# Kernel optimization log

Hardware: AMD Instinct MI355X
Metric: run time of the kernel (lower is better)

The kernel has to match this reference:

```python
import jax, jax.numpy as jnp
import numpy as np

HH, WW = 7, 7  # pooled output size (module init: height, width)


def setup_inputs() -> dict:
    key = jax.random.key(0)
    k1, k2, k3, k4, k5 = jax.random.split(key, 5)
    C, Hf, Wf = 512, 64, 256        # conv feature map (stride 8)
    B = 4096                        # number of RoI boxes
    img_h, img_w = 512, 2048        # original image size
    feats = jax.random.normal(k1, (C, Hf, Wf), dtype=jnp.float32)
    w = jax.random.uniform(k2, (B,), minval=16.0, maxval=256.0)
    h = jax.random.uniform(k3, (B,), minval=16.0, maxval=128.0)
    xc = jax.random.uniform(k4, (B,), minval=0.0, maxval=float(img_w))
    yc = jax.random.uniform(k5, (B,), minval=0.0, maxval=float(img_h))
    boxes = jnp.stack([xc, yc, w, h], axis=1).astype(jnp.float32)  # (B,4) xc,yc,w,h in image coords
    return {"feats": feats, "boxes": boxes, "img_height": img_h, "img_width": img_w}


def _bilinear_sample(feats, px, py):
    """feats: (C,Hf,Wf); px,py: (B,HH,WW) pixel coords in feature map. Zero padding outside."""
    C, Hf, Wf = feats.shape
    x0 = jnp.floor(px)
    y0 = jnp.floor(py)
    x1 = x0 + 1.0
    y1 = y0 + 1.0
    wx1 = px - x0
    wx0 = 1.0 - wx1
    wy1 = py - y0
    wy0 = 1.0 - wy1

    def gather(xi, yi):
        valid = (xi >= 0) & (xi <= Wf - 1) & (yi >= 0) & (yi <= Hf - 1)
        xi_c = jnp.clip(xi, 0, Wf - 1).astype(jnp.int32)
        yi_c = jnp.clip(yi, 0, Hf - 1).astype(jnp.int32)
        v = feats[:, yi_c, xi_c]                     # (C,B,HH,WW)
        return v * valid[None].astype(feats.dtype)

    out = (gather(x0, y0) * (wx0 * wy0)[None]
           + gather(x1, y0) * (wx1 * wy0)[None]
           + gather(x0, y1) * (wx0 * wy1)[None]
           + gather(x1, y1) * (wx1 * wy1)[None])    # (C,B,HH,WW)
    return jnp.transpose(out, (1, 0, 2, 3))          # (B,C,HH,WW)


def reference(feats, boxes, img_height, img_width):
    # box_to_affine (densecap BoxToAffine, align_corners=True normalization) fused
    # with affine_grid: sample coords computed inline per box.
    B = boxes.shape[0]
    C, Hf, Wf = feats.shape
    xc, yc, w, h = boxes[:, 0], boxes[:, 1], boxes[:, 2], boxes[:, 3]
    tx = jnp.linspace(-1.0, 1.0, WW, dtype=feats.dtype)
    ty = jnp.linspace(-1.0, 1.0, HH, dtype=feats.dtype)
    inv_w = 1.0 / (img_width - 1)
    inv_h = 1.0 / (img_height - 1)
    # normalized image coords: gx = (2*xc-(W-1))/(W-1) + tx * w/(W-1)
    gx = (2.0 * xc[:, None] - (img_width - 1)) * inv_w + (w * inv_w)[:, None] * tx[None, :]   # (B,WW)
    gy = (2.0 * yc[:, None] - (img_height - 1)) * inv_h + (h * inv_h)[:, None] * ty[None, :]  # (B,HH)
    # map normalized [-1,1] to feature-map pixel coords (align_corners=True)
    px = (gx + 1.0) * 0.5 * (Wf - 1)
    py = (gy + 1.0) * 0.5 * (Hf - 1)
    px = jnp.broadcast_to(px[:, None, :], (B, HH, WW))
    py = jnp.broadcast_to(py[:, :, None], (B, HH, WW))
    return _bilinear_sample(feats, px, py)            # (B,C,HH,WW)
```

## Files before the change

### kernel.cpp

```cpp
#include <hip/hip_runtime.h>
#include <math.h>

#define HH 7
#define WW 7
#define CC 512
#define HF 64
#define WF 256
#define NS 49
#define CHUNK 128
#define ROWS4 (CC / 4)
#define NE4 ((CHUNK * NS) / 4)
#define NBINS 2048

typedef float floatv4 __attribute__((ext_vector_type(4)));

__global__ __launch_bounds__(256) void transpose_feats(const float* __restrict__ in,
                                                       float* __restrict__ out) {
    __shared__ float tile[32][33];
    const int P = HF * WF;
    int p  = blockIdx.x * 32 + threadIdx.x;
    int cb = blockIdx.y * 32;
#pragma unroll
    for (int r = 0; r < 32; r += 8)
        tile[threadIdx.y + r][threadIdx.x] = in[(size_t)(cb + threadIdx.y + r) * P + p];
    __syncthreads();
    int c  = cb + threadIdx.x;
    int pb = blockIdx.x * 32;
#pragma unroll
    for (int r = 0; r < 32; r += 8)
        out[(size_t)(pb + threadIdx.y + r) * CC + c] = tile[threadIdx.x][threadIdx.y + r];
}

__device__ __forceinline__ int box_key(const float* __restrict__ boxes, int b,
                                       float sy, float sx) {
    float xc = boxes[b * 4 + 0];
    float yc = boxes[b * 4 + 1];
    int yb = (int)(yc * sy);
    int xb = (int)(xc * sx);
    yb = min(max(yb, 0), 31);
    xb = min(max(xb, 0), 63);
    if (yb & 1) xb = 63 - xb;
    return (yb << 6) | xb;
}

__global__ __launch_bounds__(256) void sort_boxes(const float* __restrict__ boxes,
                                                  const int* __restrict__ ih_p,
                                                  const int* __restrict__ iw_p,
                                                  int B, int* __restrict__ perm) {
    __shared__ int hist[NBINS];
    __shared__ int part[256];
    const int tid = threadIdx.x;
    const float sy = 32.0f / (float)ih_p[0];
    const float sx = 64.0f / (float)iw_p[0];

    for (int i = tid; i < NBINS; i += 256) hist[i] = 0;
    __syncthreads();
    for (int b = tid; b < B; b += 256)
        atomicAdd(&hist[box_key(boxes, b, sy, sx)], 1);
    __syncthreads();
    const int base = tid * (NBINS / 256);
    int s = 0;
#pragma unroll
    for (int i = 0; i < NBINS / 256; ++i) { int v = hist[base + i]; hist[base + i] = s; s += v; }
    part[tid] = s;
    __syncthreads();
    if (tid == 0) {
        int acc = 0;
        for (int t = 0; t < 256; ++t) { int v = part[t]; part[t] = acc; acc += v; }
    }
    __syncthreads();
    const int off = part[tid];
#pragma unroll
    for (int i = 0; i < NBINS / 256; ++i) hist[base + i] += off;
    __syncthreads();
    for (int b = tid; b < B; b += 256) {
        int pos = atomicAdd(&hist[box_key(boxes, b, sy, sx)], 1);
        perm[pos] = b;
    }
}

__device__ __forceinline__ void box_setup(int s, int b,
                                          const float* __restrict__ boxes,
                                          const int* __restrict__ ih_p,
                                          const int* __restrict__ iw_p,
                                          int4* o_out, float4* w_out) {
    int i = s / WW;
    int j = s - i * WW;
    float IW1 = (float)(iw_p[0] - 1);
    float IH1 = (float)(ih_p[0] - 1);
    float xc = boxes[b * 4 + 0];
    float yc = boxes[b * 4 + 1];
    float bw = boxes[b * 4 + 2];
    float bh = boxes[b * 4 + 3];
    float inv_w = 1.0f / IW1;
    float inv_h = 1.0f / IH1;
    float tx = (float)(j - 3) * (1.0f / 3.0f);
    float ty = (float)(i - 3) * (1.0f / 3.0f);
    float gx = (2.0f * xc - IW1) * inv_w + (bw * inv_w) * tx;
    float gy = (2.0f * yc - IH1) * inv_h + (bh * inv_h) * ty;
    float px = (gx + 1.0f) * 0.5f * (float)(WF - 1);
    float py = (gy + 1.0f) * 0.5f * (float)(HF - 1);

    float x0f = floorf(px), y0f = floorf(py);
    float wx1 = px - x0f, wx0 = 1.0f - wx1;
    float wy1 = py - y0f, wy0 = 1.0f - wy1;
    float x1f = x0f + 1.0f, y1f = y0f + 1.0f;

    bool vx0 = (x0f >= 0.0f) && (x0f <= (float)(WF - 1));
    bool vx1 = (x1f >= 0.0f) && (x1f <= (float)(WF - 1));
    bool vy0 = (y0f >= 0.0f) && (y0f <= (float)(HF - 1));
    bool vy1 = (y1f >= 0.0f) && (y1f <= (float)(HF - 1));

    int xi0 = (int)fminf(fmaxf(x0f, 0.0f), (float)(WF - 1));
    int xi1 = (int)fminf(fmaxf(x1f, 0.0f), (float)(WF - 1));
    int yi0 = (int)fminf(fmaxf(y0f, 0.0f), (float)(HF - 1));
    int yi1 = (int)fminf(fmaxf(y1f, 0.0f), (float)(HF - 1));

    int4 o;
    o.x = yi0 * WF + xi0;
    o.y = yi0 * WF + xi1;
    o.z = yi1 * WF + xi0;
    o.w = yi1 * WF + xi1;
    float4 w4;
    w4.x = wx0 * wy0 * ((vx0 && vy0) ? 1.0f : 0.0f);
    w4.y = wx1 * wy0 * ((vx1 && vy0) ? 1.0f : 0.0f);
    w4.z = wx0 * wy1 * ((vx0 && vy1) ? 1.0f : 0.0f);
    w4.w = wx1 * wy1 * ((vx1 && vy1) ? 1.0f : 0.0f);
    *o_out = o;
    *w_out = w4;
}

__global__ __launch_bounds__(256) void roi_pool_v4(const float* __restrict__ src,
                                                   const float* __restrict__ boxes,
                                                   const int* __restrict__ ih_p,
                                                   const int* __restrict__ iw_p,
                                                   const int* __restrict__ perm,
                                                   float* __restrict__ out) {
    __shared__ int4   s_off[NS];
    __shared__ float4 s_wt[NS];
    __shared__ float  tile[CHUNK * 64];

    const int nwg  = gridDim.x;
    const int bid  = blockIdx.x;
    const int q    = nwg >> 3, r = nwg & 7;
    const int xcd  = bid & 7, slot = bid >> 3;
    const int rank = xcd * q + min(xcd, r) + slot;
    const int b    = perm[rank];

    const int tid = threadIdx.x;
    const int g   = tid & 31;
    const int h   = tid >> 5;

    if (tid < NS) {
        int4 o; float4 w4;
        box_setup(tid, b, boxes, ih_p, iw_p, &o, &w4);
        o.x *= ROWS4; o.y *= ROWS4; o.z *= ROWS4; o.w *= ROWS4;
        s_off[tid] = o;
        s_wt[tid]  = w4;
    }
    __syncthreads();

    int4   o_r[7];
    float4 w_r[7];
    int    sig_r[7];
#pragma unroll
    for (int it = 0; it < 7; ++it) {
        int s = h + (it << 3);
        if (s < NS) {
            o_r[it]   = s_off[s];
            w_r[it]   = s_wt[s];
            sig_r[it] = (s >> 2) | ((s & 3) << 4);
        }
    }

    const size_t outbase = (size_t)b * (CC * NS);
    const float4* src4   = (const float4*)src;

    for (int c0 = 0; c0 < CC; c0 += CHUNK) {
        const int cb4 = c0 >> 2;
#pragma unroll
        for (int it = 0; it < 7; ++it) {
            int s = h + (it << 3);
            if (s < NS) {
                int4   o = o_r[it];
                float4 w = w_r[it];
                float4 a  = src4[o.x + cb4 + g];
                float4 bb = src4[o.y + cb4 + g];
                float4 c  = src4[o.z + cb4 + g];
                float4 d  = src4[o.w + cb4 + g];
                int base = g << 8;
                int sw   = sig_r[it] ^ g;
                tile[base +       sw] = a.x * w.x + bb.x * w.y + c.x * w.z + d.x * w.w;
                tile[base +  64 + sw] = a.y * w.x + bb.y * w.y + c.y * w.z + d.y * w.w;
                tile[base + 128 + sw] = a.z * w.x + bb.z * w.y + c.z * w.z + d.z * w.w;
                tile[base + 192 + sw] = a.w * w.x + bb.w * w.y + c.w * w.z + d.w * w.w;
            }
        }
        __syncthreads();
        float* outc = out + outbase + (size_t)c0 * NS;
        for (int k4 = tid; k4 < NE4; k4 += 256) {
            int e = k4 << 2;
            int c = e / NS;
            int s = e - c * NS;
            floatv4 v;
            v.x = tile[(c << 6) + (((s >> 2) | ((s & 3) << 4)) ^ (c >> 2))];
            if (++s == NS) { s = 0; ++c; }
            v.y = tile[(c << 6) + (((s >> 2) | ((s & 3) << 4)) ^ (c >> 2))];
            if (++s == NS) { s = 0; ++c; }
            v.z = tile[(c << 6) + (((s >> 2) | ((s & 3) << 4)) ^ (c >> 2))];
            if (++s == NS) { s = 0; ++c; }
            v.w = tile[(c << 6) + (((s >> 2) | ((s & 3) << 4)) ^ (c >> 2))];
            __builtin_nontemporal_store(v, (floatv4*)outc + k4);
        }
        __syncthreads();
    }
}

__global__ __launch_bounds__(256) void roi_pool_fb(const float* __restrict__ src,
                                                   const float* __restrict__ boxes,
                                                   const int* __restrict__ ih_p,
                                                   const int* __restrict__ iw_p,
                                                   float* __restrict__ out) {
    __shared__ int4   s_off[NS];
    __shared__ float4 s_wt[NS];
    __shared__ float  tile[NS * 257];

    const int b   = blockIdx.x;
    const int tid = threadIdx.x;

    if (tid < NS) {
        int4 o; float4 w4;
        box_setup(tid, b, boxes, ih_p, iw_p, &o, &w4);
        s_off[tid] = o;
        s_wt[tid]  = w4;
    }
    __syncthreads();

    const size_t outbase = (size_t)b * (CC * NS);
    for (int c0 = 0; c0 < CC; c0 += 256) {
        const int cterm = (c0 + tid) * (HF * WF);
        for (int s = 0; s < NS; ++s) {
            int4   o = s_off[s];
            float4 w = s_wt[s];
            float v = src[o.x + cterm] * w.x + src[o.y + cterm] * w.y +
                      src[o.z + cterm] * w.z + src[o.w + cterm] * w.w;
            tile[s * 257 + tid] = v;
        }
        __syncthreads();
        const size_t ob = outbase + (size_t)c0 * NS;
        for (int k = tid; k < 256 * NS; k += 256) {
            int cl = k / NS;
            int s  = k - cl * NS;
            out[ob + k] = tile[s * 257 + cl];
        }
        __syncthreads();
    }
}

extern "C" void kernel_launch(void* const* d_in, const int* in_sizes, int n_in,
                              void* d_out, int out_size, void* d_ws, size_t ws_size,
                              hipStream_t stream) {
    const float* feats = (const float*)d_in[0];
    const float* boxes = (const float*)d_in[1];
    const int*   ih    = (const int*)d_in[2];
    const int*   iw    = (const int*)d_in[3];
    float*       out   = (float*)d_out;
    const int B = in_sizes[1] / 4;

    const size_t tf_bytes = (size_t)CC * HF * WF * sizeof(float);
    const size_t need = tf_bytes + (size_t)B * sizeof(int);
    if (ws_size >= need) {
        float* tf   = (float*)d_ws;
        int*   perm = (int*)((char*)d_ws + tf_bytes);
        dim3 tb(32, 8);
        dim3 tg((HF * WF) / 32, CC / 32);
        transpose_feats<<<tg, tb, 0, stream>>>(feats, tf);
        sort_boxes<<<1, 256, 0, stream>>>(boxes, ih, iw, B, perm);
        roi_pool_v4<<<B, 256, 0, stream>>>(tf, boxes, ih, iw, perm, out);
    } else {
        roi_pool_fb<<<B, 256, 0, stream>>>(feats, boxes, ih, iw, out);
    }
}
```

Before: 473.5 us.

## Deduplicate bilinear source cells per box and stage them in LDS

The pooling kernel now computes the separable x/y sample coordinates once per axis, sorts and dedups the distinct feature rows and columns, and loads each unique (y,x) cell's channel vector into LDS only once per 32-channel chunk. Each output element is then interpolated from LDS using per-sample cell indices and weights, instead of issuing four global gathers per sample. This cuts redundant global loads when samples share neighbouring pixels, at the cost of extra serial setup (insertion sorts on single threads), more LDS reads per output and more barrier-separated chunks. The sort kernel's serial prefix over partial sums is also replaced with a parallel Hillis-Steele scan.

```diff
diff --git a/kernel.cpp b/kernel.cpp
--- a/kernel.cpp
+++ b/kernel.cpp
@@ -7,9 +7,10 @@
 #define HF 64
 #define WF 256
 #define NS 49
-#define CHUNK 128
-#define ROWS4 (CC / 4)
-#define NE4 ((CHUNK * NS) / 4)
+#define MAXC 196
+#define CSTR 40
+#define CH 32
+#define NP4 ((CH * NS) / 4)
 #define NBINS 2048
 
 typedef float floatv4 __attribute__((ext_vector_type(4)));
@@ -64,12 +65,13 @@
     for (int i = 0; i < NBINS / 256; ++i) { int v = hist[base + i]; hist[base + i] = s; s += v; }
     part[tid] = s;
     __syncthreads();
-    if (tid == 0) {
-        int acc = 0;
-        for (int t = 0; t < 256; ++t) { int v = part[t]; part[t] = acc; acc += v; }
-    }
-    __syncthreads();
-    const int off = part[tid];
+    for (int d = 1; d < 256; d <<= 1) {
+        int v = (tid >= d) ? part[tid - d] : 0;
+        __syncthreads();
+        part[tid] += v;
+        __syncthreads();
+    }
+    const int off = part[tid] - s;
 #pragma unroll
     for (int i = 0; i < NBINS / 256; ++i) hist[base + i] += off;
     __syncthreads();
@@ -130,15 +132,20 @@
     *w_out = w4;
 }
 
-__global__ __launch_bounds__(256) void roi_pool_v4(const float* __restrict__ src,
+__global__ __launch_bounds__(256) void roi_pool_v5(const float* __restrict__ src,
                                                    const float* __restrict__ boxes,
                                                    const int* __restrict__ ih_p,
                                                    const int* __restrict__ iw_p,
                                                    const int* __restrict__ perm,
                                                    float* __restrict__ out) {
-    __shared__ int4   s_off[NS];
+    __shared__ int    xs_l[14], ys_l[14];
+    __shared__ int    rx_l[7][2], ry_l[7][2];
+    __shared__ float  wxf[7][2], wyf[7][2];
+    __shared__ int    s_nx, s_ny;
+    __shared__ int    cell_off4[MAXC];
+    __shared__ int4   s_kq[NS];
     __shared__ float4 s_wt[NS];
-    __shared__ float  tile[CHUNK * 64];
+    __shared__ float  cell_lds[MAXC * CSTR];
 
     const int nwg  = gridDim.x;
     const int bid  = blockIdx.x;
@@ -146,70 +153,135 @@
     const int xcd  = bid & 7, slot = bid >> 3;
     const int rank = xcd * q + min(xcd, r) + slot;
     const int b    = perm[rank];
-
-    const int tid = threadIdx.x;
-    const int g   = tid & 31;
-    const int h   = tid >> 5;
+    const int tid  = threadIdx.x;
+
+    if (tid < 7) {
+        float IW1 = (float)(iw_p[0] - 1);
+        float IH1 = (float)(ih_p[0] - 1);
+        float xc = boxes[b * 4 + 0], yc = boxes[b * 4 + 1];
+        float bw = boxes[b * 4 + 2], bh = boxes[b * 4 + 3];
+        float t  = (float)(tid - 3) * (1.0f / 3.0f);
+
+        float gx  = (2.0f * xc - IW1) / IW1 + (bw / IW1) * t;
+        float px  = (gx + 1.0f) * 0.5f * (float)(WF - 1);
+        float x0f = floorf(px);
+        float wx1 = px - x0f, wx0 = 1.0f - wx1;
+        bool vx0 = (x0f >= 0.0f) && (x0f <= (float)(WF - 1));
+        bool vx1 = (x0f + 1.0f >= 0.0f) && (x0f + 1.0f <= (float)(WF - 1));
+        int xi0 = (int)fminf(fmaxf(x0f, 0.0f), (float)(WF - 1));
+        int xi1 = (int)fminf(fmaxf(x0f + 1.0f, 0.0f), (float)(WF - 1));
+        xs_l[2 * tid] = xi0; xs_l[2 * tid + 1] = xi1;
+        rx_l[tid][0] = xi0;  rx_l[tid][1] = xi1;
+        wxf[tid][0] = wx0 * (vx0 ? 1.0f : 0.0f);
+        wxf[tid][1] = wx1 * (vx1 ? 1.0f : 0.0f);
+
+        float gy  = (2.0f * yc - IH1) / IH1 + (bh / IH1) * t;
+        float py  = (gy + 1.0f) * 0.5f * (float)(HF - 1);
+        float y0f = floorf(py);
+        float wy1v = py - y0f, wy0v = 1.0f - wy1v;
+        bool vy0 = (y0f >= 0.0f) && (y0f <= (float)(HF - 1));
+        bool vy1 = (y0f + 1.0f >= 0.0f) && (y0f + 1.0f <= (float)(HF - 1));
+        int yi0 = (int)fminf(fmaxf(y0f, 0.0f), (float)(HF - 1));
+        int yi1 = (int)fminf(fmaxf(y0f + 1.0f, 0.0f), (float)(HF - 1));
+        ys_l[2 * tid] = yi0; ys_l[2 * tid + 1] = yi1;
+        ry_l[tid][0] = yi0;  ry_l[tid][1] = yi1;
+        wyf[tid][0] = wy0v * (vy0 ? 1.0f : 0.0f);
+        wyf[tid][1] = wy1v * (vy1 ? 1.0f : 0.0f);
+    }
+    __syncthreads();
+
+    if (tid == 0) {
+        for (int a = 1; a < 14; ++a) { int v = xs_l[a]; int p2 = a;
+            while (p2 > 0 && xs_l[p2 - 1] > v) { xs_l[p2] = xs_l[p2 - 1]; --p2; }
+            xs_l[p2] = v; }
+        int m = 1;
+        for (int a = 1; a < 14; ++a) if (xs_l[a] != xs_l[m - 1]) xs_l[m++] = xs_l[a];
+        s_nx = m;
+    }
+    if (tid == 64) {
+        for (int a = 1; a < 14; ++a) { int v = ys_l[a]; int p2 = a;
+            while (p2 > 0 && ys_l[p2 - 1] > v) { ys_l[p2] = ys_l[p2 - 1]; --p2; }
+            ys_l[p2] = v; }
+        int m = 1;
+        for (int a = 1; a < 14; ++a) if (ys_l[a] != ys_l[m - 1]) ys_l[m++] = ys_l[a];
+        s_ny = m;
+    }
+    __syncthreads();
+    const int nx = s_nx, ny = s_ny;
+    const int nc = nx * ny;
+
+    if (tid < 7) {
+#pragma unroll
+        for (int d = 0; d < 2; ++d) {
+            int v = rx_l[tid][d]; int idx = 0;
+            for (int a = 0; a < nx; ++a) if (xs_l[a] == v) idx = a;
+            rx_l[tid][d] = idx;
+            v = ry_l[tid][d]; idx = 0;
+            for (int a = 0; a < ny; ++a) if (ys_l[a] == v) idx = a;
+            ry_l[tid][d] = idx;
+        }
+    }
+    for (int k = tid; k < nc; k += 256) {
+        int ky = k / nx, kx = k - ky * nx;
+        cell_off4[k] = (ys_l[ky] * WF + xs_l[kx]) * (CC / 4);
+    }
+    __syncthreads();
 
     if (tid < NS) {
-        int4 o; float4 w4;
-        box_setup(tid, b, boxes, ih_p, iw_p, &o, &w4);
-        o.x *= ROWS4; o.y *= ROWS4; o.z *= ROWS4; o.w *= ROWS4;
-        s_off[tid] = o;
-        s_wt[tid]  = w4;
-    }
-    __syncthreads();
-
-    int4   o_r[7];
-    float4 w_r[7];
-    int    sig_r[7];
-#pragma unroll
-    for (int it = 0; it < 7; ++it) {
-        int s = h + (it << 3);
-        if (s < NS) {
-            o_r[it]   = s_off[s];
-            w_r[it]   = s_wt[s];
-            sig_r[it] = (s >> 2) | ((s & 3) << 4);
-        }
-    }
+        int i = tid / 7, j = tid - i * 7;
+        int r0 = ry_l[i][0] * nx, r1 = ry_l[i][1] * nx;
+        int c0i = rx_l[j][0], c1i = rx_l[j][1];
+        s_kq[tid] = make_int4(r0 + c0i, r0 + c1i, r1 + c0i, r1 + c1i);
+        float wx0 = wxf[j][0], wx1 = wxf[j][1];
+        float wy0 = wyf[i][0], wy1 = wyf[i][1];
+        s_wt[tid] = make_float4(wx0 * wy0, wx1 * wy0, wx0 * wy1, wx1 * wy1);
+    }
+    __syncthreads();
 
     const size_t outbase = (size_t)b * (CC * NS);
     const float4* src4   = (const float4*)src;
-
-    for (int c0 = 0; c0 < CC; c0 += CHUNK) {
-        const int cb4 = c0 >> 2;
-#pragma unroll
-        for (int it = 0; it < 7; ++it) {
-            int s = h + (it << 3);
-            if (s < NS) {
-                int4   o = o_r[it];
-                float4 w = w_r[it];
-                float4 a  = src4[o.x + cb4 + g];
-                float4 bb = src4[o.y + cb4 + g];
-                float4 c  = src4[o.z + cb4 + g];
-                float4 d  = src4[o.w + cb4 + g];
-                int base = g << 8;
-                int sw   = sig_r[it] ^ g;
-                tile[base +       sw] = a.x * w.x + bb.x * w.y + c.x * w.z + d.x * w.w;
-                tile[base +  64 + sw] = a.y * w.x + bb.y * w.y + c.y * w.z + d.y * w.w;
-                tile[base + 128 + sw] = a.z * w.x + bb.z * w.y + c.z * w.z + d.z * w.w;
-                tile[base + 192 + sw] = a.w * w.x + bb.w * w.y + c.w * w.z + d.w * w.w;
-            }
-        }
-        __syncthreads();
-        float* outc = out + outbase + (size_t)c0 * NS;
-        for (int k4 = tid; k4 < NE4; k4 += 256) {
+    const int iters = (nc + 31) >> 5;
+
+    for (int cc = 0; cc < CC / CH; ++cc) {
+        const int c04 = cc << 3;
+        for (int it = 0; it < iters; ++it) {
+            int k = (it << 5) + (tid >> 3);
+            if (k < nc) {
+                int p = tid & 7;
+                float4 v = src4[cell_off4[k] + c04 + p];
+                *(float4*)&cell_lds[k * CSTR + (p << 2)] = v;
+            }
+        }
+        __syncthreads();
+        float* outc = out + outbase + (size_t)(cc * CH) * NS;
+        for (int k4 = tid; k4 < NP4; k4 += 256) {
             int e = k4 << 2;
             int c = e / NS;
             int s = e - c * NS;
             floatv4 v;
-            v.x = tile[(c << 6) + (((s >> 2) | ((s & 3) << 4)) ^ (c >> 2))];
+            {
+                int4 qd = s_kq[s]; float4 w = s_wt[s];
+                v.x = cell_lds[qd.x * CSTR + c] * w.x + cell_lds[qd.y * CSTR + c] * w.y
+                    + cell_lds[qd.z * CSTR + c] * w.z + cell_lds[qd.w * CSTR + c] * w.w;
+            }
             if (++s == NS) { s = 0; ++c; }
-            v.y = tile[(c << 6) + (((s >> 2) | ((s & 3) << 4)) ^ (c >> 2))];
+            {
+                int4 qd = s_kq[s]; float4 w = s_wt[s];
+                v.y = cell_lds[qd.x * CSTR + c] * w.x + cell_lds[qd.y * CSTR + c] * w.y
+                    + cell_lds[qd.z * CSTR + c] * w.z + cell_lds[qd.w * CSTR + c] * w.w;
+            }
             if (++s == NS) { s = 0; ++c; }
-            v.z = tile[(c << 6) + (((s >> 2) | ((s & 3) << 4)) ^ (c >> 2))];
+            {
+                int4 qd = s_kq[s]; float4 w = s_wt[s];
+                v.z = cell_lds[qd.x * CSTR + c] * w.x + cell_lds[qd.y * CSTR + c] * w.y
+                    + cell_lds[qd.z * CSTR + c] * w.z + cell_lds[qd.w * CSTR + c] * w.w;
+            }
             if (++s == NS) { s = 0; ++c; }
-            v.w = tile[(c << 6) + (((s >> 2) | ((s & 3) << 4)) ^ (c >> 2))];
+            {
+                int4 qd = s_kq[s]; float4 w = s_wt[s];
+                v.w = cell_lds[qd.x * CSTR + c] * w.x + cell_lds[qd.y * CSTR + c] * w.y
+                    + cell_lds[qd.z * CSTR + c] * w.z + cell_lds[qd.w * CSTR + c] * w.w;
+            }
             __builtin_nontemporal_store(v, (floatv4*)outc + k4);
         }
         __syncthreads();
@@ -276,7 +348,7 @@
         dim3 tg((HF * WF) / 32, CC / 32);
         transpose_feats<<<tg, tb, 0, stream>>>(feats, tf);
         sort_boxes<<<1, 256, 0, stream>>>(boxes, ih, iw, B, perm);
-        roi_pool_v4<<<B, 256, 0, stream>>>(tf, boxes, ih, iw, perm, out);
+        roi_pool_v5<<<B, 256, 0, stream>>>(tf, boxes, ih, iw, perm, out);
     } else {
         roi_pool_fb<<<B, 256, 0, stream>>>(feats, boxes, ih, iw, out);
     }
```

Measured after the change: 685.4 us. +44.8%, slower.

## Split single-block box sort into multi-block histogram, scan and scatter kernels

Applied to the files above, without the earlier changes.

Replaces the one-block counting sort of boxes with four kernels: zero a global histogram, count keys with global atomics across many blocks, scan it with a single-block parallel Hillis-Steele scan, then scatter permutation indices across many blocks. The aim is to stop the serial single-block sort, including its one-thread prefix loop, from sitting on the critical path before the pooling kernel. The cost is three extra kernel launches and global rather than shared-memory atomics. The order of boxes within each bin becomes nondeterministic, which only affects processing order and not the output.

```diff
diff --git a/kernel.cpp b/kernel.cpp
--- a/kernel.cpp
+++ b/kernel.cpp
@@ -43,37 +43,52 @@
     return (yb << 6) | xb;
 }
 
-__global__ __launch_bounds__(256) void sort_boxes(const float* __restrict__ boxes,
+__global__ __launch_bounds__(256) void hist_zero(int* __restrict__ hist) {
+    hist[blockIdx.x * 256 + threadIdx.x] = 0;
+}
+
+__global__ __launch_bounds__(256) void hist_count(const float* __restrict__ boxes,
                                                   const int* __restrict__ ih_p,
                                                   const int* __restrict__ iw_p,
-                                                  int B, int* __restrict__ perm) {
-    __shared__ int hist[NBINS];
+                                                  int B, int* __restrict__ hist) {
+    int b = blockIdx.x * 256 + threadIdx.x;
+    if (b < B) {
+        float sy = 32.0f / (float)ih_p[0];
+        float sx = 64.0f / (float)iw_p[0];
+        atomicAdd(&hist[box_key(boxes, b, sy, sx)], 1);
+    }
+}
+
+__global__ __launch_bounds__(256) void hist_scan(int* __restrict__ hist) {
     __shared__ int part[256];
-    const int tid = threadIdx.x;
-    const float sy = 32.0f / (float)ih_p[0];
-    const float sx = 64.0f / (float)iw_p[0];
-
-    for (int i = tid; i < NBINS; i += 256) hist[i] = 0;
-    __syncthreads();
-    for (int b = tid; b < B; b += 256)
-        atomicAdd(&hist[box_key(boxes, b, sy, sx)], 1);
-    __syncthreads();
+    const int tid  = threadIdx.x;
     const int base = tid * (NBINS / 256);
+    int v[NBINS / 256];
     int s = 0;
 #pragma unroll
-    for (int i = 0; i < NBINS / 256; ++i) { int v = hist[base + i]; hist[base + i] = s; s += v; }
+    for (int i = 0; i < NBINS / 256; ++i) { v[i] = s; s += hist[base + i]; }
     part[tid] = s;
     __syncthreads();
-    if (tid == 0) {
-        int acc = 0;
-        for (int t = 0; t < 256; ++t) { int v = part[t]; part[t] = acc; acc += v; }
-    }
-    __syncthreads();
-    const int off = part[tid];
-#pragma unroll
-    for (int i = 0; i < NBINS / 256; ++i) hist[base + i] += off;
-    __syncthreads();
-    for (int b = tid; b < B; b += 256) {
+    for (int d = 1; d < 256; d <<= 1) {
+        int t = (tid >= d) ? part[tid - d] : 0;
+        __syncthreads();
+        part[tid] += t;
+        __syncthreads();
+    }
+    const int off = part[tid] - s;
+#pragma unroll
+    for (int i = 0; i < NBINS / 256; ++i) hist[base + i] = v[i] + off;
+}
+
+__global__ __launch_bounds__(256) void scatter_perm(const float* __restrict__ boxes,
+                                                    const int* __restrict__ ih_p,
+                                                    const int* __restrict__ iw_p,
+                                                    int B, int* __restrict__ hist,
+                                                    int* __restrict__ perm) {
+    int b = blockIdx.x * 256 + threadIdx.x;
+    if (b < B) {
+        float sy = 32.0f / (float)ih_p[0];
+        float sx = 64.0f / (float)iw_p[0];
         int pos = atomicAdd(&hist[box_key(boxes, b, sy, sx)], 1);
         perm[pos] = b;
     }
@@ -268,14 +283,18 @@
     const int B = in_sizes[1] / 4;
 
     const size_t tf_bytes = (size_t)CC * HF * WF * sizeof(float);
-    const size_t need = tf_bytes + (size_t)B * sizeof(int);
+    const size_t need = tf_bytes + (size_t)B * sizeof(int) + (size_t)NBINS * sizeof(int);
     if (ws_size >= need) {
         float* tf   = (float*)d_ws;
         int*   perm = (int*)((char*)d_ws + tf_bytes);
+        int*   hist = (int*)((char*)d_ws + tf_bytes + (size_t)B * sizeof(int));
         dim3 tb(32, 8);
         dim3 tg((HF * WF) / 32, CC / 32);
         transpose_feats<<<tg, tb, 0, stream>>>(feats, tf);
-        sort_boxes<<<1, 256, 0, stream>>>(boxes, ih, iw, B, perm);
+        hist_zero<<<NBINS / 256, 256, 0, stream>>>(hist);
+        hist_count<<<(B + 255) / 256, 256, 0, stream>>>(boxes, ih, iw, B, hist);
+        hist_scan<<<1, 256, 0, stream>>>(hist);
+        scatter_perm<<<(B + 255) / 256, 256, 0, stream>>>(boxes, ih, iw, B, hist, perm);
         roi_pool_v4<<<B, 256, 0, stream>>>(tf, boxes, ih, iw, perm, out);
     } else {
         roi_pool_fb<<<B, 256, 0, stream>>>(feats, boxes, ih, iw, out);
```

Result: no change. 465.1 us (-1.8%).
